# Kernel optimization log

Measured on AMD Instinct MI355X. Metric: run time of the kernel, lower is better.

## Reference

```python
import jax, jax.numpy as jnp
import numpy as np

L, B, T, D, H = 8, 4, 1024, 1024, 16
DH = D // H
TPB, NB = 16, 64  # tokens_per_block, max_blocks; T == TPB*NB
EPS = 1e-5


def _block_causal_mask():
    idx = jnp.arange(T)
    causal = idx[:, None] >= idx[None, :]
    blk = idx // TPB
    block_diag = blk[:, None] == blk[None, :]
    return causal | block_diag  # [T, T] bool


def _ln(x, g, b):
    mu = jnp.mean(x, axis=-1, keepdims=True)
    var = jnp.mean(jnp.square(x - mu), axis=-1, keepdims=True)
    return (x - mu) * jax.lax.rsqrt(var + EPS) * g + b


def setup_inputs() -> dict:
    key = jax.random.key(0)
    ks = jax.random.split(key, 8)
    s = 0.02
    inp = {
        'sequences': jax.random.normal(ks[0], (B, T, D), jnp.float32),
        'Wq': jax.random.normal(ks[1], (L, D, D), jnp.float32) * s,
        'bq': jnp.zeros((L, D), jnp.float32),
        'Wk': jax.random.normal(ks[2], (L, D, D), jnp.float32) * s,
        'bk': jnp.zeros((L, D), jnp.float32),
        'Wv': jax.random.normal(ks[3], (L, D, D), jnp.float32) * s,
        'bv': jnp.zeros((L, D), jnp.float32),
        'Wp': jax.random.normal(ks[4], (L, D, D), jnp.float32) * s,
        'bp': jnp.zeros((L, D), jnp.float32),
        'ln1_g': jnp.ones((L, D), jnp.float32),
        'ln1_b': jnp.zeros((L, D), jnp.float32),
        'ln2_g': jnp.ones((L, D), jnp.float32),
        'ln2_b': jnp.zeros((L, D), jnp.float32),
        'W1': jax.random.normal(ks[5], (L, D, 4 * D), jnp.float32) * s,
        'b1': jnp.zeros((L, 4 * D), jnp.float32),
        'W2': jax.random.normal(ks[6], (L, 4 * D, D), jnp.float32) * s,
        'b2': jnp.zeros((L, D), jnp.float32),
        'lnf_g': jnp.ones((D,), jnp.float32),
        'lnf_b': jnp.zeros((D,), jnp.float32),
    }
    return inp


def reference(sequences, Wq, bq, Wk, bk, Wv, bv, Wp, bp,
              ln1_g, ln1_b, ln2_g, ln2_b, W1, b1, W2, b2, lnf_g, lnf_b):
    mask = _block_causal_mask()
    scale = 1.0 / np.sqrt(DH)
    x = sequences
    for i in range(L):
        h = _ln(x, ln1_g[i], ln1_b[i])
        q = (h @ Wq[i] + bq[i]).reshape(B, T, H, DH)
        k = (h @ Wk[i] + bk[i]).reshape(B, T, H, DH)
        v = (h @ Wv[i] + bv[i]).reshape(B, T, H, DH)
        att = jnp.einsum('bthd,bshd->bhts', q, k) * scale  # [B,H,T,T]
        att = jnp.where(mask, att, -jnp.inf)
        att = jax.nn.softmax(att, axis=-1)
        y = jnp.einsum('bhts,bshd->bthd', att, v).reshape(B, T, D)
        x = x + (y @ Wp[i] + bp[i])
        h2 = _ln(x, ln2_g[i], ln2_b[i])
        ff = jax.nn.gelu(h2 @ W1[i] + b1[i], approximate=False) @ W2[i] + b2[i]
        x = x + ff
    return _ln(x, lnf_g, lnf_b)
```

## Files before the change

### kernel.cpp

```cpp
#include <hip/hip_runtime.h>
#include <hip/hip_bf16.h>
#include <math.h>

#define B_ 4
#define T_ 1024
#define D_ 1024
#define H_ 16
#define DH_ 64
#define M_ 4096
#define QSTR_ 3072
#define EPS_ 1e-5f

typedef __attribute__((ext_vector_type(4))) float f32x4;
typedef __attribute__((ext_vector_type(8))) short s16x8;

#if __has_builtin(__builtin_amdgcn_exp2f)
#define EXP2F __builtin_amdgcn_exp2f
#else
#define EXP2F exp2f
#endif

__device__ __forceinline__ float gelu_f(float x) {
  return 0.5f * x * (1.0f + erff(x * 0.70710678118654752f));
}
__device__ __forceinline__ float b2f(unsigned short u) {
  union { unsigned int i; float f; } c; c.i = ((unsigned int)u) << 16; return c.f;
}
__device__ __forceinline__ unsigned short f2b(float f) {
  __hip_bfloat16 h = __float2bfloat16(f);
  return *reinterpret_cast<unsigned short*>(&h);
}
__device__ __forceinline__ void g2l16(void* l, const void* g) {
  __builtin_amdgcn_global_load_lds(
      (const __attribute__((address_space(1))) void*)g,
      (__attribute__((address_space(3))) void*)l, 16, 0, 0);
}

template<bool BF16OUT>
__global__ __launch_bounds__(256) void ln_kernel(
    const float* __restrict__ in, void* __restrict__ out,
    const float* __restrict__ g, const float* __restrict__ b) {
  const int row = blockIdx.x;
  const int tid = threadIdx.x;
  const float* rp = in + (size_t)row * D_;
  float4 v = *reinterpret_cast<const float4*>(rp + tid * 4);
  float s = v.x + v.y + v.z + v.w;
  float s2 = v.x * v.x + v.y * v.y + v.z * v.z + v.w * v.w;
#pragma unroll
  for (int off = 1; off < 64; off <<= 1) {
    s += __shfl_xor(s, off);
    s2 += __shfl_xor(s2, off);
  }
  __shared__ float red[2][4];
  const int wid = tid >> 6;
  if ((tid & 63) == 0) { red[0][wid] = s; red[1][wid] = s2; }
  __syncthreads();
  s = red[0][0] + red[0][1] + red[0][2] + red[0][3];
  s2 = red[1][0] + red[1][1] + red[1][2] + red[1][3];
  const float mu = s * (1.0f / D_);
  const float var = s2 * (1.0f / D_) - mu * mu;
  const float rs = rsqrtf(var + EPS_);
  float4 gv = *reinterpret_cast<const float4*>(g + tid * 4);
  float4 bv = *reinterpret_cast<const float4*>(b + tid * 4);
  float o0 = (v.x - mu) * rs * gv.x + bv.x;
  float o1 = (v.y - mu) * rs * gv.y + bv.y;
  float o2 = (v.z - mu) * rs * gv.z + bv.z;
  float o3 = (v.w - mu) * rs * gv.w + bv.w;
  if (BF16OUT) {
    ushort4 pk;
    pk.x = f2b(o0); pk.y = f2b(o1); pk.z = f2b(o2); pk.w = f2b(o3);
    *reinterpret_cast<ushort4*>((unsigned short*)out + (size_t)row * D_ + tid * 4) = pk;
  } else {
    *reinterpret_cast<float4*>((float*)out + (size_t)row * D_ + tid * 4) =
        make_float4(o0, o1, o2, o3);
  }
}

__global__ __launch_bounds__(256) void concat_bias(
    const float* __restrict__ bq, const float* __restrict__ bk,
    const float* __restrict__ bv, float* __restrict__ out) {
  const int i = blockIdx.x * 256 + threadIdx.x;
  const int l = i / QSTR_, c = i % QSTR_;
  const float* src = (c < 1024) ? bq : ((c < 2048) ? bk : bv);
  out[i] = src[l * 1024 + (c & 1023)];
}

__device__ __forceinline__ void transpose_tile(
    const float* __restrict__ src, int sld,
    __hip_bfloat16* __restrict__ dst, int dld, int k0, int n0) {
  __shared__ float tile[32][33];
  const int t = threadIdx.x;
  const int r = t >> 3;
  const int cq = (t & 7) * 4;
  float4 vv = *reinterpret_cast<const float4*>(src + (size_t)(k0 + r) * sld + n0 + cq);
  tile[r][cq + 0] = vv.x; tile[r][cq + 1] = vv.y;
  tile[r][cq + 2] = vv.z; tile[r][cq + 3] = vv.w;
  __syncthreads();
  ushort4 o;
  o.x = f2b(tile[cq + 0][r]); o.y = f2b(tile[cq + 1][r]);
  o.z = f2b(tile[cq + 2][r]); o.w = f2b(tile[cq + 3][r]);
  *reinterpret_cast<ushort4*>((unsigned short*)dst + (size_t)(n0 + r) * dld + k0 + cq) = o;
}

struct TrAll {
  const float *wq, *wk, *wv, *wp, *w1, *w2;
  __hip_bfloat16 *dqkv, *dp, *d1, *d2;
};

__global__ __launch_bounds__(256) void transpose_all(TrAll a) {
  const int t = blockIdx.x;
  const float* src;
  __hip_bfloat16* dst;
  int sld, dld, k0, n0;
  if (t < 4096) {
    const int m = t >> 10, tile = t & 1023;
    k0 = (tile >> 5) * 32; n0 = (tile & 31) * 32;
    src = (m == 0) ? a.wq : (m == 1) ? a.wk : (m == 2) ? a.wv : a.wp;
    sld = 1024; dld = 1024;
    dst = (m < 3) ? (a.dqkv + (size_t)m * 1024 * 1024) : a.dp;
  } else if (t < 8192) {
    const int tile = t - 4096;
    k0 = (tile & 31) * 32; n0 = (tile >> 5) * 32;
    src = a.w1; sld = 4096; dst = a.d1; dld = 1024;
  } else {
    const int tile = t - 8192;
    k0 = (tile >> 5) * 32; n0 = (tile & 31) * 32;
    src = a.w2; sld = 1024; dst = a.d2; dld = 4096;
  }
  transpose_tile(src, sld, dst, dld, k0, n0);
}

template<int MODE, int BN>
__global__ __launch_bounds__(256) void gemm_mfma(
    const __hip_bfloat16* __restrict__ A,
    const __hip_bfloat16* __restrict__ Bt,
    const float* __restrict__ bias,
    void* __restrict__ Cout, int N, int K) {
  __shared__ short As[2][128 * 32];
  __shared__ short Bs[2][BN * 32];
  int bid = blockIdx.y * gridDim.x + blockIdx.x;
  const int nwg = gridDim.x * gridDim.y;
  bid = (bid & 7) * (nwg >> 3) + (bid >> 3);
  const int gn = (bid % gridDim.x) * BN;
  const int gm = (bid / gridDim.x) * 128;

  const int tid = threadIdx.x;
  const int wid = tid >> 6, lane = tid & 63;
  constexpr int MR = (BN == 128) ? 4 : 2;
  const int wm = (BN == 128) ? (wid >> 1) : wid;
  const int wn = (BN == 128) ? (wid & 1) : 0;
  const int fr = lane & 15, kg = lane >> 4;

  const int ldr = lane >> 2;
  const int ldk = (lane & 3) * 8;
  const unsigned short* ap =
      (const unsigned short*)A + (size_t)(gm + wid * 32 + ldr) * K + ldk;
  const unsigned short* bp =
      (const unsigned short*)Bt +
      (size_t)(gn + ((BN == 128) ? wid * 32 : wid * 16) + ldr) * K + ldk;

  {
    g2l16((char*)As[0] + (wid * 2) * 1024, ap);
    g2l16((char*)As[0] + (wid * 2 + 1) * 1024, ap + (size_t)16 * K);
    if (BN == 128) {
      g2l16((char*)Bs[0] + (wid * 2) * 1024, bp);
      g2l16((char*)Bs[0] + (wid * 2 + 1) * 1024, bp + (size_t)16 * K);
    } else {
      g2l16((char*)Bs[0] + wid * 1024, bp);
    }
    ap += 32; bp += 32;
  }
  asm volatile("s_waitcnt vmcnt(0)" ::: "memory");
  __syncthreads();

  f32x4 acc[MR][4] = {};
  int cur = 0;
  for (int kt = 0; kt < K; kt += 32) {
    if (kt + 32 < K) {
      g2l16((char*)As[cur ^ 1] + (wid * 2) * 1024, ap);
      g2l16((char*)As[cur ^ 1] + (wid * 2 + 1) * 1024, ap + (size_t)16 * K);
      if (BN == 128) {
        g2l16((char*)Bs[cur ^ 1] + (wid * 2) * 1024, bp);
        g2l16((char*)Bs[cur ^ 1] + (wid * 2 + 1) * 1024, bp + (size_t)16 * K);
      } else {
        g2l16((char*)Bs[cur ^ 1] + wid * 1024, bp);
      }
      ap += 32; bp += 32;
    }
    s16x8 af[MR], bfr[4];
#pragma unroll
    for (int m = 0; m < MR; ++m)
      af[m] = *reinterpret_cast<const s16x8*>(
          &As[cur][(wm * (16 * MR) + m * 16 + fr) * 32 + kg * 8]);
#pragma unroll
    for (int n = 0; n < 4; ++n)
      bfr[n] = *reinterpret_cast<const s16x8*>(
          &Bs[cur][(wn * 64 + n * 16 + fr) * 32 + kg * 8]);
#pragma unroll
    for (int m = 0; m < MR; ++m)
#pragma unroll
      for (int n = 0; n < 4; ++n)
        acc[m][n] = __builtin_amdgcn_mfma_f32_16x16x32_bf16(af[m], bfr[n], acc[m][n], 0, 0, 0);
    asm volatile("s_waitcnt vmcnt(0)" ::: "memory");
    __syncthreads();
    cur ^= 1;
  }

  const int r0 = gm + wm * (16 * MR);
  const int c0 = gn + wn * 64;
  float bb[4];
#pragma unroll
  for (int n = 0; n < 4; ++n)
    bb[n] = bias ? bias[c0 + n * 16 + fr] : 0.0f;
#pragma unroll
  for (int m = 0; m < MR; ++m) {
#pragma unroll
    for (int j = 0; j < 4; ++j) {
      const int row = r0 + m * 16 + kg * 4 + j;
#pragma unroll
      for (int n = 0; n < 4; ++n) {
        float val = acc[m][n][j] + bb[n];
        const size_t idx = (size_t)row * N + c0 + n * 16 + fr;
        if (MODE == 0) {
          ((unsigned short*)Cout)[idx] = f2b(val);
        } else if (MODE == 1) {
          float* cp = (float*)Cout + idx;
          *cp = *cp + val;
        } else {
          ((unsigned short*)Cout)[idx] = f2b(gelu_f(val));
        }
      }
    }
  }
}

__global__ __launch_bounds__(256) void attn_mfma(
    const __hip_bfloat16* __restrict__ qkv, __hip_bfloat16* __restrict__ yg) {
  const int qb = 7 - blockIdx.x;
  const int hh = blockIdx.y;
  const int bb = blockIdx.z;
  __shared__ short Qs[128 * 64];
  __shared__ short Ks[64 * 64];
  __shared__ short Vt[64 * 64];
  const int tid = threadIdx.x;
  const int wid = tid >> 6, lane = tid & 63;
  const int fr = lane & 15, kg = lane >> 4;
  const size_t qb_base = (size_t)bb * T_ * QSTR_ + (size_t)hh * DH_;
  const unsigned short* qgp = (const unsigned short*)qkv + qb_base;
  const unsigned short* kgp = qgp + 1024;
  const unsigned short* vgp = qgp + 2048;
  const float C = 0.125f * 1.4426950408889634f;

  {
    const int r8 = lane >> 3, cp = lane & 7;
#pragma unroll
    for (int u = 0; u < 4; ++u) {
      const int row = wid * 32 + u * 8 + r8;
      const int c16 = cp ^ (row & 7);
      g2l16((char*)Qs + (wid * 32 + u * 8) * 128,
            qgp + (size_t)(qb * 128 + row) * QSTR_ + c16 * 8);
    }
  }
  asm volatile("s_waitcnt vmcnt(0)" ::: "memory");
  __syncthreads();
  s16x8 qf[2][2];
#pragma unroll
  for (int rg = 0; rg < 2; ++rg) {
    const int row = wid * 32 + rg * 16 + fr;
    const char* rp = (const char*)Qs + row * 128;
    qf[rg][0] = *reinterpret_cast<const s16x8*>(rp + (((0 + kg) ^ (row & 7)) << 4));
    qf[rg][1] = *reinterpret_cast<const s16x8*>(rp + (((4 + kg) ^ (row & 7)) << 4));
  }

  f32x4 acco[2][4] = {};
  float m_run[2][4], l_run[2][4];
#pragma unroll
  for (int rg = 0; rg < 2; ++rg)
#pragma unroll
    for (int j = 0; j < 4; ++j) { m_run[rg][j] = -INFINITY; l_run[rg][j] = 0.f; }

  const int q16hi = qb * 8 + wid * 2 + 1;
  const int ntile = 2 * qb + 2;
  for (int kt = 0; kt < ntile; ++kt) {
    __syncthreads();
    {
      const int r8 = lane >> 3, cp = lane & 7;
#pragma unroll
      for (int u = 0; u < 2; ++u) {
        const int row = wid * 16 + u * 8 + r8;
        const int c16 = cp ^ (row & 7);
        g2l16((char*)Ks + (wid * 16 + u * 8) * 128,
              kgp + (size_t)(kt * 64 + row) * QSTR_ + c16 * 8);
      }
    }
    {
      const int kv0 = tid >> 3;
      const int d0 = (tid & 7) * 8;
      const int rot = tid & 7;
#pragma unroll
      for (int u = 0; u < 2; ++u) {
        const int kv = u * 32 + kv0;
        s16x8 sv = *reinterpret_cast<const s16x8*>(
            vgp + (size_t)(kt * 64 + kv) * QSTR_ + d0);
#pragma unroll
        for (int j = 0; j < 8; ++j) {
          const int jj = (j + rot) & 7;
          const int d = d0 + jj;
          *(short*)((char*)Vt + d * 128 + ((((kv >> 3) ^ jj) & 7) << 4) + (kv & 7) * 2) = sv[jj];
        }
      }
    }
    asm volatile("s_waitcnt vmcnt(0)" ::: "memory");
    __syncthreads();

    if (kt * 4 <= q16hi) {
      f32x4 accs[2][4] = {};
#pragma unroll
      for (int n = 0; n < 4; ++n) {
        const int row = n * 16 + fr;
        const char* rp = (const char*)Ks + row * 128;
        s16x8 kf0 = *reinterpret_cast<const s16x8*>(rp + (((0 + kg) ^ (row & 7)) << 4));
        s16x8 kf1 = *reinterpret_cast<const s16x8*>(rp + (((4 + kg) ^ (row & 7)) << 4));
#pragma unroll
        for (int rg = 0; rg < 2; ++rg) {
          accs[rg][n] = __builtin_amdgcn_mfma_f32_16x16x32_bf16(qf[rg][0], kf0, accs[rg][n], 0, 0, 0);
          accs[rg][n] = __builtin_amdgcn_mfma_f32_16x16x32_bf16(qf[rg][1], kf1, accs[rg][n], 0, 0, 0);
        }
      }
#pragma unroll
      for (int rg = 0; rg < 2; ++rg) {
        const int q16 = qb * 8 + wid * 2 + rg;
        float mloc[4] = {-3.0e38f, -3.0e38f, -3.0e38f, -3.0e38f};
#pragma unroll
        for (int n = 0; n < 4; ++n)
          if (kt * 4 + n <= q16)
#pragma unroll
            for (int j = 0; j < 4; ++j) mloc[j] = fmaxf(mloc[j], accs[rg][n][j]);
#pragma unroll
        for (int off = 1; off < 16; off <<= 1)
#pragma unroll
          for (int j = 0; j < 4; ++j) mloc[j] = fmaxf(mloc[j], __shfl_xor(mloc[j], off));
        float a_[4];
#pragma unroll
        for (int j = 0; j < 4; ++j) {
          const float mn = fmaxf(m_run[rg][j], mloc[j]);
          a_[j] = EXP2F((m_run[rg][j] - mn) * C);
          m_run[rg][j] = mn;
        }
        float psum[4] = {};
#pragma unroll
        for (int n = 0; n < 4; ++n) {
          const bool dead = (kt * 4 + n > q16);
          const int c16b = n * 2 + (fr >> 3);
#pragma unroll
          for (int j = 0; j < 4; ++j) {
            float p = dead ? 0.0f : EXP2F((accs[rg][n][j] - m_run[rg][j]) * C);
            psum[j] += p;
            const int row = wid * 32 + rg * 16 + kg * 4 + j;
            *(short*)((char*)Qs + row * 128 + (((c16b ^ (row & 7)) & 7) << 4) + (fr & 7) * 2) =
                (short)f2b(p);
          }
        }
#pragma unroll
        for (int j = 0; j < 4; ++j) l_run[rg][j] = l_run[rg][j] * a_[j] + psum[j];
#pragma unroll
        for (int dt = 0; dt < 4; ++dt)
#pragma unroll
          for (int j = 0; j < 4; ++j) acco[rg][dt][j] *= a_[j];
      }
#pragma unroll
      for (int rg = 0; rg < 2; ++rg) {
        const int prow = wid * 32 + rg * 16 + fr;
        const char* pp = (const char*)Qs + prow * 128;
#pragma unroll
        for (int kk = 0; kk < 2; ++kk) {
          const s16x8 pf = *reinterpret_cast<const s16x8*>(
              pp + ((((kk * 4 + kg) ^ (prow & 7)) & 7) << 4));
#pragma unroll
          for (int dt = 0; dt < 4; ++dt) {
            const int vrow = dt * 16 + fr;
            const s16x8 vf = *reinterpret_cast<const s16x8*>(
                (const char*)Vt + vrow * 128 + ((((kk * 4 + kg) ^ (vrow & 7)) & 7) << 4));
            acco[rg][dt] = __builtin_amdgcn_mfma_f32_16x16x32_bf16(pf, vf, acco[rg][dt], 0, 0, 0);
          }
        }
      }
    }
  }

#pragma unroll
  for (int off = 1; off < 16; off <<= 1)
#pragma unroll
    for (int rg = 0; rg < 2; ++rg)
#pragma unroll
      for (int j = 0; j < 4; ++j) l_run[rg][j] += __shfl_xor(l_run[rg][j], off);
  unsigned short* yp = (unsigned short*)yg + (size_t)bb * T_ * D_ + (size_t)hh * DH_;
#pragma unroll
  for (int rg = 0; rg < 2; ++rg) {
    float inv[4];
#pragma unroll
    for (int j = 0; j < 4; ++j) inv[j] = 1.0f / l_run[rg][j];
#pragma unroll
    for (int dt = 0; dt < 4; ++dt)
#pragma unroll
      for (int j = 0; j < 4; ++j) {
        const int row = qb * 128 + wid * 32 + rg * 16 + kg * 4 + j;
        yp[(size_t)row * D_ + dt * 16 + fr] = f2b(acco[rg][dt][j] * inv[j]);
      }
  }
}

extern "C" void kernel_launch(void* const* d_in, const int* in_sizes, int n_in,
                              void* d_out, int out_size, void* d_ws, size_t ws_size,
                              hipStream_t stream) {
  (void)in_sizes; (void)n_in; (void)out_size; (void)ws_size;
  const float* seq  = (const float*)d_in[0];
  const float* Wq   = (const float*)d_in[1];
  const float* bq   = (const float*)d_in[2];
  const float* Wk   = (const float*)d_in[3];
  const float* bk   = (const float*)d_in[4];
  const float* Wv   = (const float*)d_in[5];
  const float* bv   = (const float*)d_in[6];
  const float* Wp   = (const float*)d_in[7];
  const float* bp   = (const float*)d_in[8];
  const float* ln1g = (const float*)d_in[9];
  const float* ln1b = (const float*)d_in[10];
  const float* ln2g = (const float*)d_in[11];
  const float* ln2b = (const float*)d_in[12];
  const float* W1   = (const float*)d_in[13];
  const float* b1   = (const float*)d_in[14];
  const float* W2   = (const float*)d_in[15];
  const float* b2   = (const float*)d_in[16];
  const float* lnfg = (const float*)d_in[17];
  const float* lnfb = (const float*)d_in[18];

  float* x = (float*)d_out;
  char* ws = (char*)d_ws;
  const size_t MB = 1024ull * 1024ull;
  typedef __hip_bfloat16 bf16;
  bf16*  wtqkv = (bf16*)(ws + 0 * MB);
  bf16*  wtp   = (bf16*)(ws + 6 * MB);
  bf16*  wtF1  = (bf16*)(ws + 8 * MB);
  bf16*  wtF2  = (bf16*)(ws + 16 * MB);
  bf16*  hb    = (bf16*)(ws + 24 * MB);
  bf16*  qkv   = (bf16*)(ws + 32 * MB);
  bf16*  mid   = (bf16*)(ws + 56 * MB);
  float* bqkv  = (float*)(ws + 88 * MB);

  hipMemcpyAsync(x, seq, (size_t)M_ * D_ * sizeof(float), hipMemcpyDeviceToDevice, stream);

  const dim3 blk(256);
  concat_bias<<<96, blk, 0, stream>>>(bq, bk, bv, bqkv);

  for (int i = 0; i < 8; ++i) {
    const size_t wo  = (size_t)i * D_ * D_;
    const size_t vo  = (size_t)i * D_;
    const size_t w1o = (size_t)i * D_ * 4 * D_;

    ln_kernel<true><<<M_, blk, 0, stream>>>(x, hb, ln1g + vo, ln1b + vo);
    TrAll ta;
    ta.wq = Wq + wo; ta.wk = Wk + wo; ta.wv = Wv + wo; ta.wp = Wp + wo;
    ta.w1 = W1 + w1o; ta.w2 = W2 + w1o;
    ta.dqkv = wtqkv; ta.dp = wtp; ta.d1 = wtF1; ta.d2 = wtF2;
    transpose_all<<<12288, blk, 0, stream>>>(ta);
    gemm_mfma<0, 128><<<dim3(24, 32), blk, 0, stream>>>(
        hb, wtqkv, bqkv + (size_t)i * QSTR_, qkv, QSTR_, 1024);
    attn_mfma<<<dim3(8, 16, 4), blk, 0, stream>>>(qkv, hb);
    gemm_mfma<1, 64><<<dim3(16, 32), blk, 0, stream>>>(hb, wtp, bp + vo, x, 1024, 1024);
    ln_kernel<true><<<M_, blk, 0, stream>>>(x, hb, ln2g + vo, ln2b + vo);
    gemm_mfma<2, 128><<<dim3(32, 32), blk, 0, stream>>>(
        hb, wtF1, b1 + (size_t)i * 4096, mid, 4096, 1024);
    gemm_mfma<1, 64><<<dim3(16, 32), blk, 0, stream>>>(
        mid, wtF2, b2 + vo, x, 1024, 4096);
  }
  ln_kernel<false><<<M_, blk, 0, stream>>>(x, x, lnfg, lnfb);
}
```

Measured before the change: 2.305 ms.

## Triple-buffer GEMM LDS staging with partial vmcnt waits

Moves the bf16 MFMA GEMM from double to triple buffering of A/B tiles in LDS, issuing global-to-LDS loads two K-steps ahead. It uses partial s_waitcnt vmcnt counts so the loop waits only for the current tile instead of draining all outstanding loads every iteration. The aim is to hide global memory latency behind MFMA work. In exchange it uses 1.5x the LDS, which may reduce occupancy, and relies on hand-counted vmcnt values matching the g2l16 instruction counts.

```diff
diff --git a/kernel.cpp b/kernel.cpp
--- a/kernel.cpp
+++ b/kernel.cpp
@@ -136,8 +136,8 @@
     const __hip_bfloat16* __restrict__ Bt,
     const float* __restrict__ bias,
     void* __restrict__ Cout, int N, int K) {
-  __shared__ short As[2][128 * 32];
-  __shared__ short Bs[2][BN * 32];
+  __shared__ short As[3][128 * 32];
+  __shared__ short Bs[3][BN * 32];
   int bid = blockIdx.y * gridDim.x + blockIdx.x;
   const int nwg = gridDim.x * gridDim.y;
   bid = (bid & 7) * (nwg >> 3) + (bid >> 3);
@@ -159,52 +159,59 @@
       (const unsigned short*)Bt +
       (size_t)(gn + ((BN == 128) ? wid * 32 : wid * 16) + ldr) * K + ldk;
 
-  {
-    g2l16((char*)As[0] + (wid * 2) * 1024, ap);
-    g2l16((char*)As[0] + (wid * 2 + 1) * 1024, ap + (size_t)16 * K);
-    if (BN == 128) {
-      g2l16((char*)Bs[0] + (wid * 2) * 1024, bp);
-      g2l16((char*)Bs[0] + (wid * 2 + 1) * 1024, bp + (size_t)16 * K);
+  const int nkt = K >> 5;
+
+#define STAGE_T(t, buf)                                                    \
+  {                                                                        \
+    const unsigned short* a_ = ap + (size_t)(t) * 32;                      \
+    g2l16((char*)As[buf] + (wid * 2) * 1024, a_);                          \
+    g2l16((char*)As[buf] + (wid * 2 + 1) * 1024, a_ + (size_t)16 * K);     \
+    const unsigned short* b_ = bp + (size_t)(t) * 32;                      \
+    if (BN == 128) {                                                       \
+      g2l16((char*)Bs[buf] + (wid * 2) * 1024, b_);                        \
+      g2l16((char*)Bs[buf] + (wid * 2 + 1) * 1024, b_ + (size_t)16 * K);   \
+    } else {                                                               \
+      g2l16((char*)Bs[buf] + wid * 1024, b_);                              \
+    }                                                                      \
+  }
+
+  STAGE_T(0, 0);
+  STAGE_T(1, 1);
+
+  f32x4 acc[MR][4] = {};
+  for (int t = 0; t < nkt; ++t) {
+    const int buf = t % 3;
+    if (t + 2 < nkt) STAGE_T(t + 2, (t + 2) % 3);
+    const int rem = nkt - 1 - t;
+    if (rem >= 2) {
+      if (BN == 128) asm volatile("s_waitcnt vmcnt(8)" ::: "memory");
+      else           asm volatile("s_waitcnt vmcnt(6)" ::: "memory");
+    } else if (rem == 1) {
+      if (BN == 128) asm volatile("s_waitcnt vmcnt(4)" ::: "memory");
+      else           asm volatile("s_waitcnt vmcnt(3)" ::: "memory");
     } else {
-      g2l16((char*)Bs[0] + wid * 1024, bp);
-    }
-    ap += 32; bp += 32;
-  }
-  asm volatile("s_waitcnt vmcnt(0)" ::: "memory");
-  __syncthreads();
-
-  f32x4 acc[MR][4] = {};
-  int cur = 0;
-  for (int kt = 0; kt < K; kt += 32) {
-    if (kt + 32 < K) {
-      g2l16((char*)As[cur ^ 1] + (wid * 2) * 1024, ap);
-      g2l16((char*)As[cur ^ 1] + (wid * 2 + 1) * 1024, ap + (size_t)16 * K);
-      if (BN == 128) {
-        g2l16((char*)Bs[cur ^ 1] + (wid * 2) * 1024, bp);
-        g2l16((char*)Bs[cur ^ 1] + (wid * 2 + 1) * 1024, bp + (size_t)16 * K);
-      } else {
-        g2l16((char*)Bs[cur ^ 1] + wid * 1024, bp);
-      }
-      ap += 32; bp += 32;
-    }
+      asm volatile("s_waitcnt vmcnt(0)" ::: "memory");
+    }
+    __builtin_amdgcn_s_barrier();
+    __builtin_amdgcn_sched_barrier(0);
     s16x8 af[MR], bfr[4];
 #pragma unroll
     for (int m = 0; m < MR; ++m)
       af[m] = *reinterpret_cast<const s16x8*>(
-          &As[cur][(wm * (16 * MR) + m * 16 + fr) * 32 + kg * 8]);
+          &As[buf][(wm * (16 * MR) + m * 16 + fr) * 32 + kg * 8]);
 #pragma unroll
     for (int n = 0; n < 4; ++n)
       bfr[n] = *reinterpret_cast<const s16x8*>(
-          &Bs[cur][(wn * 64 + n * 16 + fr) * 32 + kg * 8]);
+          &Bs[buf][(wn * 64 + n * 16 + fr) * 32 + kg * 8]);
 #pragma unroll
     for (int m = 0; m < MR; ++m)
 #pragma unroll
       for (int n = 0; n < 4; ++n)
         acc[m][n] = __builtin_amdgcn_mfma_f32_16x16x32_bf16(af[m], bfr[n], acc[m][n], 0, 0, 0);
-    asm volatile("s_waitcnt vmcnt(0)" ::: "memory");
-    __syncthreads();
-    cur ^= 1;
-  }
+    __builtin_amdgcn_sched_barrier(0);
+    __builtin_amdgcn_s_barrier();
+  }
+#undef STAGE_T
 
   const int r0 = gm + wm * (16 * MR);
   const int c0 = gn + wn * 64;
```

Measured after the change: 2.324 ms. No clear change (+0.8%).
